# Performance work log

Hardware: AMD Instinct MI355X
Metric: run time of the kernel (lower is better)

Reference implementation:

```python
import jax, jax.numpy as jnp
import numpy as np

N, M = 4096, 8192
IN_DIM, OUT_DIM = 4096, 1024
NUM_SAMPLE = 10


def setup_inputs() -> dict:
    key = jax.random.key(0)
    k1, k2, k3, k4, k5 = jax.random.split(key, 5)
    node_features = jax.random.normal(k1, (N, IN_DIM), dtype=jnp.float32)
    neighbor_features = jax.random.normal(k2, (M, IN_DIM), dtype=jnp.float32)
    # Xavier-ish scale for params
    weight = jax.random.normal(k3, (OUT_DIM, IN_DIM), dtype=jnp.float32) * (1.0 / np.sqrt(IN_DIM))
    attention_vector = jax.random.normal(k4, (2 * OUT_DIM, 1), dtype=jnp.float32) * 0.05
    neighbor_idx = jax.random.randint(k5, (N, NUM_SAMPLE), 0, M, dtype=jnp.int32)
    return {
        "node_features": node_features,
        "neighbor_features": neighbor_features,
        "weight": weight,
        "attention_vector": attention_vector,
        "neighbor_idx": neighbor_idx,
    }


def reference(node_features, neighbor_features, weight, attention_vector, neighbor_idx):
    # Linear transform: [N, out], [M, out]
    node_t = node_features @ weight.T
    neigh_t = neighbor_features @ weight.T

    # combined @ attention_vector decomposes:
    # cat([h_i, h_j]) @ a == h_i @ a1 + h_j @ a2  (same math, no [N,M,2*out] tensor)
    a1 = attention_vector[:OUT_DIM, 0]   # [out]
    a2 = attention_vector[OUT_DIM:, 0]   # [out]
    scores = jax.nn.leaky_relu((node_t @ a1)[:, None] + (neigh_t @ a2)[None, :],
                               negative_slope=0.2)  # [N, M]

    # Build dense 0/1 mask from sampled neighbor indices (ragged -> dense)
    rows = jnp.arange(N, dtype=jnp.int32)[:, None]                  # [N,1]
    mask = jnp.zeros((N, M), dtype=jnp.float32).at[rows, neighbor_idx].set(1.0)

    scores = jnp.where(mask == 0, -jnp.inf, scores)
    attn = jax.nn.softmax(scores, axis=1)           # masked softmax over neighbor pool
    return attn @ neigh_t                           # [N, out]
```

## Files before the change

### kernel.cpp

```cpp
#include <hip/hip_runtime.h>

#define IN_DIM  4096
#define OUT_DIM 1024
#define NN      4096
#define MM      8192
#define NSAMP   10

typedef __bf16 bf16x8 __attribute__((ext_vector_type(8)));
typedef float  fx4    __attribute__((ext_vector_type(4)));

__device__ __forceinline__ ushort f2bf(float f) {
    union { float f; unsigned u; } v; v.f = f;
    unsigned u = v.u;
    return (ushort)((u + 0x7FFFu + ((u >> 16) & 1u)) >> 16);
}
__device__ __forceinline__ float bf2f(ushort u) {
    union { unsigned u; float f; } v; v.u = ((unsigned)u) << 16;
    return v.f;
}

#define GLDS(g, l) __builtin_amdgcn_global_load_lds(                           \
    (const __attribute__((address_space(1))) unsigned*)(g),                    \
    (__attribute__((address_space(3))) unsigned*)(l), 16, 0, 0)

__global__ __launch_bounds__(256) void k_attvec(const float* __restrict__ W,
                                                const float* __restrict__ att,
                                                float* __restrict__ v1,
                                                float* __restrict__ v2,
                                                ushort* __restrict__ Wbf) {
    int k  = blockIdx.x * 256 + threadIdx.x;
    int o0 = blockIdx.y * 128;
    float s1 = 0.f, s2 = 0.f;
    for (int o = o0; o < o0 + 128; ++o) {
        float w = W[(size_t)o * IN_DIM + k];
        Wbf[(size_t)o * IN_DIM + k] = f2bf(w);
        s1 += att[o] * w;
        s2 += att[OUT_DIM + o] * w;
    }
    atomicAdd(&v1[k], s1);
    atomicAdd(&v2[k], s2);
}

__global__ __launch_bounds__(256) void k_node_alpha(const float* __restrict__ X,
                                                    const float* __restrict__ v1,
                                                    float* __restrict__ outv) {
    int row = blockIdx.x;
    const float4* xr = reinterpret_cast<const float4*>(X + (size_t)row * IN_DIM);
    const float4* vr = reinterpret_cast<const float4*>(v1);
    float s = 0.f;
    for (int i = threadIdx.x; i < IN_DIM / 4; i += 256) {
        float4 a = xr[i], b = vr[i];
        s += a.x * b.x + a.y * b.y + a.z * b.z + a.w * b.w;
    }
    for (int off = 32; off > 0; off >>= 1) s += __shfl_down(s, off, 64);
    __shared__ float ws[4];
    if ((threadIdx.x & 63) == 0) ws[threadIdx.x >> 6] = s;
    __syncthreads();
    if (threadIdx.x == 0) outv[row] = ws[0] + ws[1] + ws[2] + ws[3];
}

__global__ __launch_bounds__(256) void k_cast_beta(const float* __restrict__ X,
                                                   const float* __restrict__ v2,
                                                   ushort* __restrict__ Xbf,
                                                   float* __restrict__ beta) {
    int row = blockIdx.x;
    const float4* xr = reinterpret_cast<const float4*>(X + (size_t)row * IN_DIM);
    const float4* vr = reinterpret_cast<const float4*>(v2);
    ushort4* yr = reinterpret_cast<ushort4*>(Xbf + (size_t)row * IN_DIM);
    float s = 0.f;
    for (int i = threadIdx.x; i < IN_DIM / 4; i += 256) {
        float4 a = xr[i], b = vr[i];
        s += a.x * b.x + a.y * b.y + a.z * b.z + a.w * b.w;
        ushort4 o;
        o.x = f2bf(a.x); o.y = f2bf(a.y); o.z = f2bf(a.z); o.w = f2bf(a.w);
        yr[i] = o;
    }
    for (int off = 32; off > 0; off >>= 1) s += __shfl_down(s, off, 64);
    __shared__ float ws[4];
    if ((threadIdx.x & 63) == 0) ws[threadIdx.x >> 6] = s;
    __syncthreads();
    if (threadIdx.x == 0) beta[row] = ws[0] + ws[1] + ws[2] + ws[3];
}

#define TM 128
#define TN 128
#define BK 32
#define KSPLIT (IN_DIM / 2)

__global__ __launch_bounds__(256, 4) void k_gemm(const ushort* __restrict__ A,
                                                 const ushort* __restrict__ B,
                                                 ushort* __restrict__ P) {
    __shared__ __align__(16) ushort As[TM * BK];
    __shared__ __align__(16) ushort Bs[TN * BK];
    const int tid  = threadIdx.x;
    const int lane = tid & 63;
    const int wave = tid >> 6;
    const int wm   = (wave >> 1) * 64;
    const int wn   = (wave & 1) * 64;
    const int bm   = blockIdx.x * TM;
    const int bn   = blockIdx.y * TN;
    const int kb   = blockIdx.z * KSPLIT;
    const int quad = lane >> 4;
    const int lrow = lane & 15;

    const int srow  = wave * 32 + (lane >> 2);
    const int skoff = (lane & 3) * 8;
    const ushort* gA = A + (size_t)(bm + srow) * IN_DIM + kb + skoff;
    const ushort* gB = B + (size_t)(bn + srow) * IN_DIM + kb + skoff;
    ushort* lA = As + wave * 1024;
    ushort* lB = Bs + wave * 1024;

    fx4 acc[4][4] = {};

    for (int k0 = 0; k0 < KSPLIT; k0 += BK) {
        GLDS(gA + k0,                lA);
        GLDS(gA + k0 + 16 * IN_DIM,  lA + 512);
        GLDS(gB + k0,                lB);
        GLDS(gB + k0 + 16 * IN_DIM,  lB + 512);
        __syncthreads();

        bf16x8 af[4], bfr[4];
#pragma unroll
        for (int mi = 0; mi < 4; ++mi)
            af[mi] = *reinterpret_cast<const bf16x8*>(As + (wm + mi * 16 + lrow) * BK + quad * 8);
#pragma unroll
        for (int ni = 0; ni < 4; ++ni)
            bfr[ni] = *reinterpret_cast<const bf16x8*>(Bs + (wn + ni * 16 + lrow) * BK + quad * 8);
#pragma unroll
        for (int mi = 0; mi < 4; ++mi)
#pragma unroll
            for (int ni = 0; ni < 4; ++ni)
                acc[mi][ni] = __builtin_amdgcn_mfma_f32_16x16x32_bf16(af[mi], bfr[ni], acc[mi][ni], 0, 0, 0);
        __syncthreads();
    }

    ushort* Pz = P + (size_t)blockIdx.z * MM * OUT_DIM;
#pragma unroll
    for (int mi = 0; mi < 4; ++mi)
#pragma unroll
        for (int ni = 0; ni < 4; ++ni) {
            int r = bm + wm + mi * 16 + quad * 4;
            int c = bn + wn + ni * 16 + lrow;
#pragma unroll
            for (int v = 0; v < 4; ++v)
                Pz[(size_t)(r + v) * OUT_DIM + c] = f2bf(acc[mi][ni][v]);
        }
}

__global__ __launch_bounds__(256) void k_aggregate(const ushort* __restrict__ P,
                                                   const float* __restrict__ nalpha,
                                                   const float* __restrict__ nbeta,
                                                   const int* __restrict__ nidx,
                                                   float* __restrict__ outp) {
    int row = blockIdx.x;
    __shared__ int   s_idx[NSAMP];
    __shared__ float s_w[NSAMP];
    __shared__ int   s_cnt;
    if (threadIdx.x == 0) {
        int   tmp[NSAMP];
        float sc[NSAMP];
        int   cnt = 0;
        float alpha = nalpha[row];
        float mx = -INFINITY;
        for (int s = 0; s < NSAMP; ++s) {
            int j = nidx[row * NSAMP + s];
            bool dup = false;
            for (int t = 0; t < cnt; ++t)
                if (tmp[t] == j) { dup = true; break; }
            if (!dup) {
                float x = alpha + nbeta[j];
                float v = x > 0.f ? x : 0.2f * x;
                tmp[cnt] = j;
                sc[cnt] = v;
                if (v > mx) mx = v;
                ++cnt;
            }
        }
        float sum = 0.f;
        for (int t = 0; t < cnt; ++t) { float e = expf(sc[t] - mx); sc[t] = e; sum += e; }
        float inv = 1.f / sum;
        for (int t = 0; t < cnt; ++t) { s_idx[t] = tmp[t]; s_w[t] = sc[t] * inv; }
        s_cnt = cnt;
    }
    __syncthreads();
    int cnt = s_cnt;
    int col = threadIdx.x * 4;
    float ax = 0.f, ay = 0.f, az = 0.f, aw = 0.f;
    for (int t = 0; t < cnt; ++t) {
        float w = s_w[t];
        size_t off = (size_t)s_idx[t] * OUT_DIM + col;
        ushort4 u0 = *reinterpret_cast<const ushort4*>(P + off);
        ushort4 u1 = *reinterpret_cast<const ushort4*>(P + (size_t)MM * OUT_DIM + off);
        ax += w * (bf2f(u0.x) + bf2f(u1.x));
        ay += w * (bf2f(u0.y) + bf2f(u1.y));
        az += w * (bf2f(u0.z) + bf2f(u1.z));
        aw += w * (bf2f(u0.w) + bf2f(u1.w));
    }
    float4 o; o.x = ax; o.y = ay; o.z = az; o.w = aw;
    *reinterpret_cast<float4*>(outp + (size_t)row * OUT_DIM + col) = o;
}

extern "C" void kernel_launch(void* const* d_in, const int* in_sizes, int n_in,
                              void* d_out, int out_size, void* d_ws, size_t ws_size,
                              hipStream_t stream) {
    const float* node_f  = (const float*)d_in[0];
    const float* neigh_f = (const float*)d_in[1];
    const float* W       = (const float*)d_in[2];
    const float* att     = (const float*)d_in[3];
    const int*   nidx    = (const int*)d_in[4];
    float* outp = (float*)d_out;

    char* ws = (char*)d_ws;
    ushort* Abf = (ushort*)ws;
    ushort* Wbf = (ushort*)(ws + 67108864);
    ushort* P   = (ushort*)(ws + 75497472);
    float*  v1     = (float*)(ws + 109051904);
    float*  v2     = v1 + IN_DIM;
    float*  nalpha = v2 + IN_DIM;
    float*  nbeta  = nalpha + NN;

    hipMemsetAsync(v1, 0, 2 * IN_DIM * sizeof(float), stream);

    k_attvec    <<<dim3(16, 8), 256, 0, stream>>>(W, att, v1, v2, Wbf);
    k_node_alpha<<<NN,          256, 0, stream>>>(node_f, v1, nalpha);
    k_cast_beta <<<MM,          256, 0, stream>>>(neigh_f, v2, Abf, nbeta);
    k_gemm      <<<dim3(MM / TM, OUT_DIM / TN, 2), 256, 0, stream>>>(Abf, Wbf, P);
    k_aggregate <<<NN,          256, 0, stream>>>(P, nalpha, nbeta, nidx, outp);
}
```

Measured before the change: 398.9 us.

## Merge row-dot kernels, widen attvec grid, parallelize softmax with lane shuffles

Merges the node-alpha and neighbor cast/beta kernels into one launch over N+M rows, which removes a launch and the tail gap between them. Doubles the attvec grid in the output dimension so twice as many blocks share the W pass. Replaces the single-thread serial dedup and softmax in the aggregation kernel with a 16-lane shuffle reduction, so duplicates get zero weight instead of being compacted out. The aggregation loop now always runs all samples, paying extra gathers for duplicated indices.

```diff
diff --git a/kernel.cpp b/kernel.cpp
--- a/kernel.cpp
+++ b/kernel.cpp
@@ -29,9 +29,9 @@
                                                 float* __restrict__ v2,
                                                 ushort* __restrict__ Wbf) {
     int k  = blockIdx.x * 256 + threadIdx.x;
-    int o0 = blockIdx.y * 128;
+    int o0 = blockIdx.y * 64;
     float s1 = 0.f, s2 = 0.f;
-    for (int o = o0; o < o0 + 128; ++o) {
+    for (int o = o0; o < o0 + 64; ++o) {
         float w = W[(size_t)o * IN_DIM + k];
         Wbf[(size_t)o * IN_DIM + k] = f2bf(w);
         s1 += att[o] * w;
@@ -41,45 +41,43 @@
     atomicAdd(&v2[k], s2);
 }
 
-__global__ __launch_bounds__(256) void k_node_alpha(const float* __restrict__ X,
-                                                    const float* __restrict__ v1,
-                                                    float* __restrict__ outv) {
+__global__ __launch_bounds__(256) void k_rows(const float* __restrict__ node_f,
+                                              const float* __restrict__ neigh_f,
+                                              const float* __restrict__ v1,
+                                              const float* __restrict__ v2,
+                                              float* __restrict__ nalpha,
+                                              float* __restrict__ nbeta,
+                                              ushort* __restrict__ Abf) {
     int row = blockIdx.x;
-    const float4* xr = reinterpret_cast<const float4*>(X + (size_t)row * IN_DIM);
-    const float4* vr = reinterpret_cast<const float4*>(v1);
     float s = 0.f;
-    for (int i = threadIdx.x; i < IN_DIM / 4; i += 256) {
-        float4 a = xr[i], b = vr[i];
-        s += a.x * b.x + a.y * b.y + a.z * b.z + a.w * b.w;
+    if (row < NN) {
+        const float4* xr = reinterpret_cast<const float4*>(node_f + (size_t)row * IN_DIM);
+        const float4* vr = reinterpret_cast<const float4*>(v1);
+        for (int i = threadIdx.x; i < IN_DIM / 4; i += 256) {
+            float4 a = xr[i], b = vr[i];
+            s += a.x * b.x + a.y * b.y + a.z * b.z + a.w * b.w;
+        }
+    } else {
+        int j = row - NN;
+        const float4* xr = reinterpret_cast<const float4*>(neigh_f + (size_t)j * IN_DIM);
+        const float4* vr = reinterpret_cast<const float4*>(v2);
+        ushort4* yr = reinterpret_cast<ushort4*>(Abf + (size_t)j * IN_DIM);
+        for (int i = threadIdx.x; i < IN_DIM / 4; i += 256) {
+            float4 a = xr[i], b = vr[i];
+            s += a.x * b.x + a.y * b.y + a.z * b.z + a.w * b.w;
+            ushort4 o;
+            o.x = f2bf(a.x); o.y = f2bf(a.y); o.z = f2bf(a.z); o.w = f2bf(a.w);
+            yr[i] = o;
+        }
     }
     for (int off = 32; off > 0; off >>= 1) s += __shfl_down(s, off, 64);
     __shared__ float ws[4];
     if ((threadIdx.x & 63) == 0) ws[threadIdx.x >> 6] = s;
     __syncthreads();
-    if (threadIdx.x == 0) outv[row] = ws[0] + ws[1] + ws[2] + ws[3];
-}
-
-__global__ __launch_bounds__(256) void k_cast_beta(const float* __restrict__ X,
-                                                   const float* __restrict__ v2,
-                                                   ushort* __restrict__ Xbf,
-                                                   float* __restrict__ beta) {
-    int row = blockIdx.x;
-    const float4* xr = reinterpret_cast<const float4*>(X + (size_t)row * IN_DIM);
-    const float4* vr = reinterpret_cast<const float4*>(v2);
-    ushort4* yr = reinterpret_cast<ushort4*>(Xbf + (size_t)row * IN_DIM);
-    float s = 0.f;
-    for (int i = threadIdx.x; i < IN_DIM / 4; i += 256) {
-        float4 a = xr[i], b = vr[i];
-        s += a.x * b.x + a.y * b.y + a.z * b.z + a.w * b.w;
-        ushort4 o;
-        o.x = f2bf(a.x); o.y = f2bf(a.y); o.z = f2bf(a.z); o.w = f2bf(a.w);
-        yr[i] = o;
-    }
-    for (int off = 32; off > 0; off >>= 1) s += __shfl_down(s, off, 64);
-    __shared__ float ws[4];
-    if ((threadIdx.x & 63) == 0) ws[threadIdx.x >> 6] = s;
-    __syncthreads();
-    if (threadIdx.x == 0) beta[row] = ws[0] + ws[1] + ws[2] + ws[3];
+    if (threadIdx.x == 0) {
+        float t = ws[0] + ws[1] + ws[2] + ws[3];
+        if (row < NN) nalpha[row] = t; else nbeta[row - NN] = t;
+    }
 }
 
 #define TM 128
@@ -155,38 +153,40 @@
     int row = blockIdx.x;
     __shared__ int   s_idx[NSAMP];
     __shared__ float s_w[NSAMP];
-    __shared__ int   s_cnt;
-    if (threadIdx.x == 0) {
-        int   tmp[NSAMP];
-        float sc[NSAMP];
-        int   cnt = 0;
-        float alpha = nalpha[row];
-        float mx = -INFINITY;
-        for (int s = 0; s < NSAMP; ++s) {
-            int j = nidx[row * NSAMP + s];
-            bool dup = false;
-            for (int t = 0; t < cnt; ++t)
-                if (tmp[t] == j) { dup = true; break; }
-            if (!dup) {
-                float x = alpha + nbeta[j];
-                float v = x > 0.f ? x : 0.2f * x;
-                tmp[cnt] = j;
-                sc[cnt] = v;
-                if (v > mx) mx = v;
-                ++cnt;
-            }
-        }
-        float sum = 0.f;
-        for (int t = 0; t < cnt; ++t) { float e = expf(sc[t] - mx); sc[t] = e; sum += e; }
-        float inv = 1.f / sum;
-        for (int t = 0; t < cnt; ++t) { s_idx[t] = tmp[t]; s_w[t] = sc[t] * inv; }
-        s_cnt = cnt;
+    if (threadIdx.x < 16) {
+        int t = threadIdx.x;
+        int j = (t < NSAMP) ? nidx[row * NSAMP + t] : -1;
+        float score = -INFINITY;
+        if (t < NSAMP) {
+            float x = nalpha[row] + nbeta[j];
+            score = x > 0.f ? x : 0.2f * x;
+        }
+        bool dup = false;
+#pragma unroll
+        for (int sIdx = 0; sIdx < NSAMP; ++sIdx) {
+            int js = __shfl(j, sIdx, 16);
+            if (sIdx < t && js == j) dup = true;
+        }
+        float mx = score;
+#pragma unroll
+        for (int off = 8; off > 0; off >>= 1) {
+            float o = __shfl_xor(mx, off, 16);
+            mx = o > mx ? o : mx;
+        }
+        float e = (t < NSAMP && !dup) ? expf(score - mx) : 0.f;
+        float sum = e;
+#pragma unroll
+        for (int off = 8; off > 0; off >>= 1) sum += __shfl_xor(sum, off, 16);
+        if (t < NSAMP) {
+            s_idx[t] = j;
+            s_w[t]   = e / sum;
+        }
     }
     __syncthreads();
-    int cnt = s_cnt;
     int col = threadIdx.x * 4;
     float ax = 0.f, ay = 0.f, az = 0.f, aw = 0.f;
-    for (int t = 0; t < cnt; ++t) {
+#pragma unroll
+    for (int t = 0; t < NSAMP; ++t) {
         float w = s_w[t];
         size_t off = (size_t)s_idx[t] * OUT_DIM + col;
         ushort4 u0 = *reinterpret_cast<const ushort4*>(P + off);
@@ -221,9 +221,8 @@
 
     hipMemsetAsync(v1, 0, 2 * IN_DIM * sizeof(float), stream);
 
-    k_attvec    <<<dim3(16, 8), 256, 0, stream>>>(W, att, v1, v2, Wbf);
-    k_node_alpha<<<NN,          256, 0, stream>>>(node_f, v1, nalpha);
-    k_cast_beta <<<MM,          256, 0, stream>>>(neigh_f, v2, Abf, nbeta);
-    k_gemm      <<<dim3(MM / TM, OUT_DIM / TN, 2), 256, 0, stream>>>(Abf, Wbf, P);
-    k_aggregate <<<NN,          256, 0, stream>>>(P, nalpha, nbeta, nidx, outp);
-}
+    k_attvec   <<<dim3(16, 16), 256, 0, stream>>>(W, att, v1, v2, Wbf);
+    k_rows     <<<NN + MM,      256, 0, stream>>>(node_f, neigh_f, v1, v2, nalpha, nbeta, Abf);
+    k_gemm     <<<dim3(MM / TM, OUT_DIM / TN, 2), 256, 0, stream>>>(Abf, Wbf, P);
+    k_aggregate<<<NN,           256, 0, stream>>>(P, nalpha, nbeta, nidx, outp);
+}
```

Result: faster. 381.1 us (-4.5%).
